# Performance work log

Measured on AMD Instinct MI355X. Metric: run time of the kernel, lower is better.

Reference implementation:

```python
import math
import jax, jax.numpy as jnp
import numpy as np
from jax.scipy.special import erf, erfinv, logsumexp

M = 250000          # number of (u, v) datapoints
P = 4               # n_phases
N_MC = 64           # MC samples per interface pair
IA, IB = np.triu_indices(P, 1)   # interface pair indices (Ia < Ib since I is increasing)
K = len(IA)                      # n_interfaces = 6
LOG2 = math.log(2.0)
LOG2PI = math.log(2.0 * math.pi)
LOG_GAMMA_3_2 = math.log(math.gamma(1.5))


def _logsinh(x):
    # numerically stable log(sinh(x)); x > 0 in all uses here
    s = jnp.abs(x)
    return -LOG2 + s + jnp.log1p(-jnp.exp(-2.0 * s))


def _log_bessel_05(x):
    # I_{1/2}(x) = sqrt(2/(pi x)) sinh(x)
    return 0.5 * LOG2 - 0.5 * jnp.log(math.pi * x) + _logsinh(x)


def setup_inputs() -> dict:
    key = jax.random.key(0)
    k0, k1, k2 = jax.random.split(key, 3)
    u = jax.random.uniform(k0, (M,), dtype=jnp.float32)                 # intensities in [0,1]
    v = jax.random.uniform(k1, (M,), dtype=jnp.float32) * 0.3 + 0.01    # gradient magnitudes > 0
    eps = jax.random.uniform(k2, (K, N_MC), dtype=jnp.float32)          # fresh MC draw per interface
    I = jnp.linspace(0.0, 1.0, P, dtype=jnp.float32)
    W = jnp.zeros((K + P,), dtype=jnp.float32)
    sigma_b = jnp.array([2.0], dtype=jnp.float32)
    sigma_n = jnp.array([0.1], dtype=jnp.float32)
    d = jnp.array([2.0], dtype=jnp.float32)
    r = jnp.array([0.05], dtype=jnp.float32)
    return {"u": u, "v": v, "eps": eps, "I": I, "W": W,
            "sigma_b": sigma_b, "sigma_n": sigma_n, "d": d, "r": r}


def reference(u, v, eps, I, W, sigma_b, sigma_n, d, r):
    sb = sigma_b[0]
    sn = sigma_n[0]
    dd = d[0]
    rho = jnp.tanh(r[0])
    sr = sn * jnp.sqrt(1.0 - rho)          # sigma_n * sqrt(1 - rho)
    s2 = sn ** 2 * (1.0 - rho)
    N = eps.shape[1]
    log_w = jax.nn.log_softmax(W)

    # interior phases: [P, M]
    interior = (LOG2 + 2.0 * jnp.log(v) - LOG_GAMMA_3_2 - 3.0 * jnp.log(sr)
                - (v / sr) ** 2 - jnp.log(sn) - 0.5 * LOG2PI
                - 0.5 * ((u - I[:, None]) / sn) ** 2)

    rows = [interior]
    log_v = jnp.log(v)
    v2 = v ** 2
    for k in range(K):  # small fixed loop over interface pairs
        Ia = I[IA[k]]
        Ib = I[IB[k]]
        x = eps[k] * 2.0 * dd * sb - dd * sb                              # [N]
        In = (erf(x / (math.sqrt(2.0) * sb)) + 1.0) * 0.5 * (Ib - Ia) + Ia  # [N]
        # log p(u | I): [N, M]
        lu = -jnp.log(sn) - 0.5 * LOG2PI - 0.5 * ((u[None, :] - In[:, None]) / sn) ** 2
        # G(I): [N]
        Gk = (Ib - Ia) / jnp.sqrt(2.0 * math.pi * sb ** 2) * jnp.exp(
            -erfinv(2.0 * (In - Ia) / (Ib - Ia) - 1.0) ** 2)
        # log p(v | I): [N, M]
        lb = _log_bessel_05(2.0 * v[None, :] * Gk[:, None] / s2)
        lv = (LOG2 - 2.0 * jnp.log(sr) + 1.5 * log_v[None, :]
              - 0.5 * jnp.log(Gk)[:, None] + lb
              - (v2[None, :] + Gk[:, None] ** 2) / s2)
        rows.append((-math.log(N) + logsumexp(lu + lv, axis=0))[None, :])

    log_p = jnp.concatenate(rows, axis=0)                 # [P + K, M]
    log_p_uv = logsumexp(log_w[:, None] + log_p, axis=0)  # [M]
    return -jnp.sum(log_p_uv) / u.shape[0]
```

## Files before the change

### kernel.cpp

```cpp
#include <hip/hip_runtime.h>
#include <math.h>

#define KN 384

__device__ float  g_hdr[24];
__device__ float4 g_tab[KN];
__device__ double g_part[1024];

__global__ __launch_bounds__(384) void prep_kernel(
    const float* __restrict__ eps, const float* __restrict__ I,
    const float* __restrict__ W, const float* __restrict__ sb_,
    const float* __restrict__ sn_, const float* __restrict__ d_,
    const float* __restrict__ r_) {
  const int IAc[6] = {0, 0, 0, 1, 1, 2};
  const int IBc[6] = {1, 2, 3, 2, 3, 3};
  int t = threadIdx.x;

  double sb = (double)sb_[0];
  double sn = (double)sn_[0];
  double dd = (double)d_[0];
  double r  = (double)r_[0];
  double rho = tanh(r);
  double s2 = sn * sn * (1.0 - rho);
  double sr = sqrt(s2);

  double wmax = -1e300;
  for (int j = 0; j < 10; ++j) wmax = fmax(wmax, (double)W[j]);
  double se = 0.0;
  for (int j = 0; j < 10; ++j) se += exp((double)W[j] - wmax);
  double lse = wmax + log(se);

  const double LOG2PI_ = 1.8378770664093453;
  const double LOG2_   = 0.6931471805599453;
  const double LGG32   = -0.12078223763524522;
  const double PI_     = 3.141592653589793;
  double Cterm = -log(sn) - 0.5 * LOG2PI_ - log(sr) - 0.5 * log(PI_);
  double Cint0 = LOG2_ - LGG32 - 3.0 * log(sr) - log(sn) - 0.5 * LOG2PI_;
  float isn = (float)(1.0 / sn);

  if (t == 0) {
    g_hdr[2] = isn;
    g_hdr[3] = (float)(1.0 / s2);
    for (int p = 0; p < 4; ++p) {
      g_hdr[8 + p]  = (float)exp((double)W[p] - lse + Cint0);
      g_hdr[12 + p] = I[p] * isn;
    }
    for (int k = 0; k < 6; ++k)
      g_hdr[16 + k] = (float)exp((double)W[4 + k] - lse + Cterm - log(64.0));
  }

  if (t < KN) {
    int k = t >> 6;
    float Ia = I[IAc[k]], Ib = I[IBc[k]];
    float e  = eps[t];
    float sbf = (float)sb, ddf = (float)dd;
    float x  = e * 2.0f * ddf * sbf - ddf * sbf;
    float y  = x / (1.4142135623730951f * sbf);
    float ey = erff(y);
    float In = (ey + 1.0f) * 0.5f * (Ib - Ia) + Ia;
    float q  = 2.0f * (In - Ia) / (Ib - Ia) - 1.0f;
    float gi = erfinvf(q);
    float G  = (Ib - Ia) / sqrtf((float)(2.0 * PI_) * sbf * sbf) * expf(-gi * gi);
    float4 tt;
    tt.x = In * isn;
    tt.y = (float)(2.0 / s2) * G;
    tt.z = (float)exp(-log((double)G) - (double)G * (double)G / s2);
    tt.w = 0.0f;
    g_tab[t] = tt;
  }
}

__global__ __launch_bounds__(256) void main_kernel(
    const float* __restrict__ u, const float* __restrict__ v, int M, int H) {
  __shared__ float4 stab[KN];
  __shared__ float  shc[24];
  __shared__ double red[256];
  int tid = threadIdx.x;

  for (int i = tid; i < KN; i += 256) stab[i] = g_tab[i];
  if (tid < 24) shc[tid] = g_hdr[tid];
  __syncthreads();

  double mysum = 0.0;
  int i0 = blockIdx.x * 256 + tid;
  if (i0 < H) {
    float isn = shc[2], inv_s2 = shc[3];
    int i1 = i0 + H;
    bool has1 = (i1 < M);
    float u0 = u[i0], v0 = v[i0];
    float u1 = has1 ? u[i1] : u0;
    float v1 = has1 ? v[i1] : v0;
    float us0 = u0 * isn, us1 = u1 * isn;
    float g0 = __expf(-v0 * v0 * inv_s2);
    float g1 = __expf(-v1 * v1 * inv_s2);

    float aint0 = 0.f, aint1 = 0.f;
#pragma unroll
    for (int p = 0; p < 4; ++p) {
      float cI = shc[12 + p], w = shc[8 + p];
      float d0 = us0 - cI, d1 = us1 - cI;
      aint0 = fmaf(w, __expf(-0.5f * d0 * d0), aint0);
      aint1 = fmaf(w, __expf(-0.5f * d1 * d1), aint1);
    }

    float aface0 = 0.f, aface1 = 0.f;
#pragma unroll 1
    for (int k = 0; k < 6; ++k) {
      const float4* tk = stab + (k << 6);
      float S0 = 0.f, S1 = 0.f;
#pragma unroll 8
      for (int n = 0; n < 64; ++n) {
        float4 tt = tk[n];
        float z0  = v0 * tt.y;
        float du0 = us0 - tt.x;
        float a0  = -0.5f * du0;
        float e0p = __expf(fmaf(du0, a0, z0));
        float e0m = __expf(fmaf(du0, a0, -z0));
        S0 = fmaf(tt.z, e0p - e0m, S0);
        float z1  = v1 * tt.y;
        float du1 = us1 - tt.x;
        float a1  = -0.5f * du1;
        float e1p = __expf(fmaf(du1, a1, z1));
        float e1m = __expf(fmaf(du1, a1, -z1));
        S1 = fmaf(tt.z, e1p - e1m, S1);
      }
      float wk = shc[16 + k];
      aface0 = fmaf(wk, S0, aface0);
      aface1 = fmaf(wk, S1, aface1);
    }

    float acc0 = v0 * g0 * fmaf(v0, aint0, aface0);
    float acc1 = v1 * g1 * fmaf(v1, aint1, aface1);
    mysum = (double)__logf(acc0);
    if (has1) mysum += (double)__logf(acc1);
  }

  red[tid] = mysum;
  __syncthreads();
  for (int s = 128; s > 0; s >>= 1) {
    if (tid < s) red[tid] += red[tid + s];
    __syncthreads();
  }
  if (tid == 0) g_part[blockIdx.x] = red[0];
}

__global__ __launch_bounds__(1024) void finish_kernel(float* __restrict__ out,
                                                      int nb, int M) {
  __shared__ double red[1024];
  int t = threadIdx.x;
  double s = 0.0;
  for (int i = t; i < nb; i += 1024) s += g_part[i];
  red[t] = s;
  __syncthreads();
  for (int k = 512; k > 0; k >>= 1) {
    if (t < k) red[t] += red[t + k];
    __syncthreads();
  }
  if (t == 0) out[0] = (float)(-red[0] / (double)M);
}

extern "C" void kernel_launch(void* const* d_in, const int* in_sizes, int n_in,
                              void* d_out, int out_size, void* d_ws, size_t ws_size,
                              hipStream_t stream) {
  const float* u   = (const float*)d_in[0];
  const float* v   = (const float*)d_in[1];
  const float* eps = (const float*)d_in[2];
  const float* I   = (const float*)d_in[3];
  const float* W   = (const float*)d_in[4];
  const float* sb  = (const float*)d_in[5];
  const float* sn  = (const float*)d_in[6];
  const float* dd  = (const float*)d_in[7];
  const float* r   = (const float*)d_in[8];
  int M = in_sizes[0];
  int H = (M + 1) / 2;
  int nb = (H + 255) / 256;

  hipLaunchKernelGGL(prep_kernel, dim3(1), dim3(384), 0, stream,
                     eps, I, W, sb, sn, dd, r);
  hipLaunchKernelGGL(main_kernel, dim3(nb), dim3(256), 0, stream, u, v, M, H);
  hipLaunchKernelGGL(finish_kernel, dim3(1), dim3(1024), 0, stream,
                     (float*)d_out, nb, M);
}
```

Before: 116.1 us.

## Fuse prep, main and finish kernels into one with last-block reduction

Measured after the change: 110.0 us. -5.2%, faster.

```diff
diff --git a/kernel.cpp b/kernel.cpp
--- a/kernel.cpp
+++ b/kernel.cpp
@@ -2,161 +2,139 @@
 #include <math.h>
 
 #define KN 384
+#define TPB 256
 
-__device__ float  g_hdr[24];
-__device__ float4 g_tab[KN];
 __device__ double g_part[1024];
+__device__ int    g_ctr = 0;
 
-__global__ __launch_bounds__(384) void prep_kernel(
+__global__ __launch_bounds__(TPB) void fused_kernel(
+    const float* __restrict__ u, const float* __restrict__ v,
     const float* __restrict__ eps, const float* __restrict__ I,
     const float* __restrict__ W, const float* __restrict__ sb_,
     const float* __restrict__ sn_, const float* __restrict__ d_,
-    const float* __restrict__ r_) {
+    const float* __restrict__ r_, float* __restrict__ out,
+    int M, int nb) {
+  __shared__ float4 stab[KN];
+  __shared__ double red[TPB];
+  __shared__ int    slast;
+  const int tid = threadIdx.x;
+  const int i   = blockIdx.x * TPB + tid;
+
+  float uu = 0.f, vv = 1.f;
+  if (i < M) { uu = u[i]; vv = v[i]; }
+
+  const float sb  = sb_[0];
+  const float sn  = sn_[0];
+  const float dd  = d_[0];
+  const float rho = tanhf(r_[0]);
+  const float s2  = sn * sn * (1.f - rho);
+  const float sr  = sqrtf(s2);
+  const float isn = 1.f / sn;
+  const float inv_s2 = 1.f / s2;
+
+  float wmax = W[0];
+  for (int j = 1; j < 10; ++j) wmax = fmaxf(wmax, W[j]);
+  float se = 0.f;
+  for (int j = 0; j < 10; ++j) se += expf(W[j] - wmax);
+  const float lse = wmax + logf(se);
+
+  const float LOG2PI_ = 1.8378770664093453f;
+  const float LOG2_   = 0.6931471805599453f;
+  const float LGG32   = -0.12078223763524522f;
+  const float LOGPI_  = 1.1447298858494002f;
+  const float Cterm = -logf(sn) - 0.5f * LOG2PI_ - logf(sr) - 0.5f * LOGPI_;
+  const float Cint0 = LOG2_ - LGG32 - 3.f * logf(sr) - logf(sn) - 0.5f * LOG2PI_;
+
+  float wint[4], cI[4];
+#pragma unroll
+  for (int p = 0; p < 4; ++p) {
+    wint[p] = expf(W[p] - lse + Cint0);
+    cI[p]   = I[p] * isn;
+  }
+
   const int IAc[6] = {0, 0, 0, 1, 1, 2};
   const int IBc[6] = {1, 2, 3, 2, 3, 3};
-  int t = threadIdx.x;
-
-  double sb = (double)sb_[0];
-  double sn = (double)sn_[0];
-  double dd = (double)d_[0];
-  double r  = (double)r_[0];
-  double rho = tanh(r);
-  double s2 = sn * sn * (1.0 - rho);
-  double sr = sqrt(s2);
-
-  double wmax = -1e300;
-  for (int j = 0; j < 10; ++j) wmax = fmax(wmax, (double)W[j]);
-  double se = 0.0;
-  for (int j = 0; j < 10; ++j) se += exp((double)W[j] - wmax);
-  double lse = wmax + log(se);
-
-  const double LOG2PI_ = 1.8378770664093453;
-  const double LOG2_   = 0.6931471805599453;
-  const double LGG32   = -0.12078223763524522;
-  const double PI_     = 3.141592653589793;
-  double Cterm = -log(sn) - 0.5 * LOG2PI_ - log(sr) - 0.5 * log(PI_);
-  double Cint0 = LOG2_ - LGG32 - 3.0 * log(sr) - log(sn) - 0.5 * LOG2PI_;
-  float isn = (float)(1.0 / sn);
-
-  if (t == 0) {
-    g_hdr[2] = isn;
-    g_hdr[3] = (float)(1.0 / s2);
-    for (int p = 0; p < 4; ++p) {
-      g_hdr[8 + p]  = (float)exp((double)W[p] - lse + Cint0);
-      g_hdr[12 + p] = I[p] * isn;
-    }
-    for (int k = 0; k < 6; ++k)
-      g_hdr[16 + k] = (float)exp((double)W[4 + k] - lse + Cterm - log(64.0));
-  }
-
-  if (t < KN) {
-    int k = t >> 6;
-    float Ia = I[IAc[k]], Ib = I[IBc[k]];
-    float e  = eps[t];
-    float sbf = (float)sb, ddf = (float)dd;
-    float x  = e * 2.0f * ddf * sbf - ddf * sbf;
-    float y  = x / (1.4142135623730951f * sbf);
-    float ey = erff(y);
-    float In = (ey + 1.0f) * 0.5f * (Ib - Ia) + Ia;
-    float q  = 2.0f * (In - Ia) / (Ib - Ia) - 1.0f;
-    float gi = erfinvf(q);
-    float G  = (Ib - Ia) / sqrtf((float)(2.0 * PI_) * sbf * sbf) * expf(-gi * gi);
+  for (int t = tid; t < KN; t += TPB) {
+    const int k = t >> 6;
+    const float Ia = I[IAc[k]], Ib = I[IBc[k]];
+    const float wk = expf(W[4 + k] - lse + Cterm) * (1.0f / 64.0f);
+    const float e  = eps[t];
+    const float x  = e * 2.f * dd * sb - dd * sb;
+    const float y  = x / (1.4142135623730951f * sb);
+    const float In = (erff(y) + 1.f) * 0.5f * (Ib - Ia) + Ia;
+    const float q  = 2.f * (In - Ia) / (Ib - Ia) - 1.f;
+    const float gi = erfinvf(q);
+    const float G  = (Ib - Ia) * 0.3989422804014327f / sb * expf(-gi * gi);
     float4 tt;
     tt.x = In * isn;
-    tt.y = (float)(2.0 / s2) * G;
-    tt.z = (float)exp(-log((double)G) - (double)G * (double)G / s2);
-    tt.w = 0.0f;
-    g_tab[t] = tt;
+    tt.y = 2.f * inv_s2 * G;
+    tt.z = wk * expf(-G * G * inv_s2) / G;
+    tt.w = 0.f;
+    stab[t] = tt;
   }
-}
-
-__global__ __launch_bounds__(256) void main_kernel(
-    const float* __restrict__ u, const float* __restrict__ v, int M, int H) {
-  __shared__ float4 stab[KN];
-  __shared__ float  shc[24];
-  __shared__ double red[256];
-  int tid = threadIdx.x;
-
-  for (int i = tid; i < KN; i += 256) stab[i] = g_tab[i];
-  if (tid < 24) shc[tid] = g_hdr[tid];
   __syncthreads();
 
   double mysum = 0.0;
-  int i0 = blockIdx.x * 256 + tid;
-  if (i0 < H) {
-    float isn = shc[2], inv_s2 = shc[3];
-    int i1 = i0 + H;
-    bool has1 = (i1 < M);
-    float u0 = u[i0], v0 = v[i0];
-    float u1 = has1 ? u[i1] : u0;
-    float v1 = has1 ? v[i1] : v0;
-    float us0 = u0 * isn, us1 = u1 * isn;
-    float g0 = __expf(-v0 * v0 * inv_s2);
-    float g1 = __expf(-v1 * v1 * inv_s2);
+  if (i < M) {
+    const float us = uu * isn;
+    const float g  = __expf(-vv * vv * inv_s2);
 
-    float aint0 = 0.f, aint1 = 0.f;
+    float aint = 0.f;
 #pragma unroll
     for (int p = 0; p < 4; ++p) {
-      float cI = shc[12 + p], w = shc[8 + p];
-      float d0 = us0 - cI, d1 = us1 - cI;
-      aint0 = fmaf(w, __expf(-0.5f * d0 * d0), aint0);
-      aint1 = fmaf(w, __expf(-0.5f * d1 * d1), aint1);
+      const float d0 = us - cI[p];
+      aint = fmaf(wint[p], __expf(-0.5f * d0 * d0), aint);
     }
 
-    float aface0 = 0.f, aface1 = 0.f;
-#pragma unroll 1
-    for (int k = 0; k < 6; ++k) {
-      const float4* tk = stab + (k << 6);
-      float S0 = 0.f, S1 = 0.f;
+    float aface = 0.f;
 #pragma unroll 8
-      for (int n = 0; n < 64; ++n) {
-        float4 tt = tk[n];
-        float z0  = v0 * tt.y;
-        float du0 = us0 - tt.x;
-        float a0  = -0.5f * du0;
-        float e0p = __expf(fmaf(du0, a0, z0));
-        float e0m = __expf(fmaf(du0, a0, -z0));
-        S0 = fmaf(tt.z, e0p - e0m, S0);
-        float z1  = v1 * tt.y;
-        float du1 = us1 - tt.x;
-        float a1  = -0.5f * du1;
-        float e1p = __expf(fmaf(du1, a1, z1));
-        float e1m = __expf(fmaf(du1, a1, -z1));
-        S1 = fmaf(tt.z, e1p - e1m, S1);
-      }
-      float wk = shc[16 + k];
-      aface0 = fmaf(wk, S0, aface0);
-      aface1 = fmaf(wk, S1, aface1);
+    for (int n = 0; n < KN; ++n) {
+      const float4 tt = stab[n];
+      const float z  = vv * tt.y;
+      const float du = us - tt.x;
+      const float m  = -0.5f * du;
+      const float e1 = __expf(fmaf(du, m, z));
+      const float e2 = __expf(fmaf(du, m, -z));
+      aface = fmaf(tt.z, e1 - e2, aface);
     }
 
-    float acc0 = v0 * g0 * fmaf(v0, aint0, aface0);
-    float acc1 = v1 * g1 * fmaf(v1, aint1, aface1);
-    mysum = (double)__logf(acc0);
-    if (has1) mysum += (double)__logf(acc1);
+    const float acc = vv * g * fmaf(vv, aint, aface);
+    mysum = (double)__logf(acc);
   }
 
   red[tid] = mysum;
   __syncthreads();
-  for (int s = 128; s > 0; s >>= 1) {
+  for (int s = TPB / 2; s > 0; s >>= 1) {
     if (tid < s) red[tid] += red[tid + s];
     __syncthreads();
   }
-  if (tid == 0) g_part[blockIdx.x] = red[0];
-}
+  if (tid == 0)
+    __hip_atomic_store(&g_part[blockIdx.x], red[0], __ATOMIC_RELAXED,
+                       __HIP_MEMORY_SCOPE_AGENT);
 
-__global__ __launch_bounds__(1024) void finish_kernel(float* __restrict__ out,
-                                                      int nb, int M) {
-  __shared__ double red[1024];
-  int t = threadIdx.x;
-  double s = 0.0;
-  for (int i = t; i < nb; i += 1024) s += g_part[i];
-  red[t] = s;
+  if (tid == 0) {
+    const int c = __hip_atomic_fetch_add(&g_ctr, 1, __ATOMIC_ACQ_REL,
+                                         __HIP_MEMORY_SCOPE_AGENT);
+    slast = (c == nb - 1) ? 1 : 0;
+  }
   __syncthreads();
-  for (int k = 512; k > 0; k >>= 1) {
-    if (t < k) red[t] += red[t + k];
+  if (slast) {
+    double s = 0.0;
+    for (int j = tid; j < nb; j += TPB)
+      s += __hip_atomic_load(&g_part[j], __ATOMIC_RELAXED,
+                             __HIP_MEMORY_SCOPE_AGENT);
+    red[tid] = s;
     __syncthreads();
+    for (int k2 = TPB / 2; k2 > 0; k2 >>= 1) {
+      if (tid < k2) red[tid] += red[tid + k2];
+      __syncthreads();
+    }
+    if (tid == 0) {
+      out[0] = (float)(-red[0] / (double)M);
+      __hip_atomic_store(&g_ctr, 0, __ATOMIC_RELAXED,
+                         __HIP_MEMORY_SCOPE_AGENT);
+    }
   }
-  if (t == 0) out[0] = (float)(-red[0] / (double)M);
 }
 
 extern "C" void kernel_launch(void* const* d_in, const int* in_sizes, int n_in,
@@ -171,13 +149,9 @@
   const float* sn  = (const float*)d_in[6];
   const float* dd  = (const float*)d_in[7];
   const float* r   = (const float*)d_in[8];
-  int M = in_sizes[0];
-  int H = (M + 1) / 2;
-  int nb = (H + 255) / 256;
+  const int M  = in_sizes[0];
+  const int nb = (M + TPB - 1) / TPB;
 
-  hipLaunchKernelGGL(prep_kernel, dim3(1), dim3(384), 0, stream,
-                     eps, I, W, sb, sn, dd, r);
-  hipLaunchKernelGGL(main_kernel, dim3(nb), dim3(256), 0, stream, u, v, M, H);
-  hipLaunchKernelGGL(finish_kernel, dim3(1), dim3(1024), 0, stream,
-                     (float*)d_out, nb, M);
+  hipLaunchKernelGGL(fused_kernel, dim3(nb), dim3(TPB), 0, stream,
+                     u, v, eps, I, W, sb, sn, dd, r, (float*)d_out, M, nb);
 }
```
